# Performance work log

Hardware: AMD Instinct MI355X
Metric: run time of the kernel (lower is better)

## Reference

```python
import jax, jax.numpy as jnp
import numpy as np

NUM_HEADS = 4
EPS = 1e-12  # torch F.normalize eps


def _l2norm(t):
    # normalize along last axis, matching torch.nn.functional.normalize
    n = jnp.sqrt(jnp.sum(t * t, axis=-1, keepdims=True))
    return t / jnp.maximum(n, EPS)


def setup_inputs() -> dict:
    key = jax.random.key(0)
    k1, k2 = jax.random.split(key)
    B, N, C = 4, 8192, 768
    x = jax.random.normal(k1, (B, N, C), dtype=jnp.float32)
    W_qkvv = jax.random.normal(k2, (3 * C, C), dtype=jnp.float32) * (C ** -0.5)
    temperature = jnp.ones((NUM_HEADS, 1, 1), dtype=jnp.float32)
    return {"x": x, "W_qkvv": W_qkvv, "temperature": temperature}


def reference(x, W_qkvv, temperature):
    B, N, C = x.shape
    H = NUM_HEADS
    D = C // H
    # qkvv projection: [B,N,3C] -> [3,B,H,N,D]
    qkvv = (x @ W_qkvv.T).reshape(B, N, 3, H, D).transpose(2, 0, 3, 1, 4)
    q, k, v = qkvv[0], qkvv[1], qkvv[2]        # each [B,H,N,D]
    q = jnp.swapaxes(q, -2, -1)                # [B,H,D,N]
    k = jnp.swapaxes(k, -2, -1)                # [B,H,D,N]
    v = jnp.swapaxes(v, -2, -1)                # [B,H,D,N]
    q = _l2norm(q)
    k = _l2norm(k)
    # channel attention scores: [B,H,D,D], temperature broadcast per head
    attn = jnp.einsum('bhdn,bhen->bhde', q, k) * temperature[None]
    attn = jax.nn.softmax(attn, axis=-1)
    # dropout is identity in eval mode
    x_CA = jnp.einsum('bhde,bhen->bhdn', attn, v)   # [B,H,D,N]
    out = x_CA.transpose(0, 3, 1, 2).reshape(B, N, C)
    return out
```

## Files before the change

### kernel.cpp

```cpp
#include <hip/hip_runtime.h>
#include <hip/hip_bf16.h>
#include <cstddef>
#include <cstdint>

#define B_   4
#define N_   8192
#define C_   768
#define H_   4
#define D_   192
#define CQ_  2304
#define M_   32768

typedef __attribute__((ext_vector_type(8))) short short8_t;
typedef __attribute__((ext_vector_type(4))) float f32x4;

typedef const __attribute__((address_space(1))) uint gq_uint;
typedef __attribute__((address_space(3))) uint lds_uint;

__device__ inline ushort f2bf(float f){
  uint u = __float_as_uint(f);
  u += 0x7FFFu + ((u >> 16) & 1u);
  return (ushort)(u >> 16);
}
__device__ inline float bf2f(ushort u){ return __uint_as_float(((uint)u) << 16); }

__global__ __launch_bounds__(256) void cvt_all(const float* __restrict__ x,
                                               ushort* __restrict__ xb,
                                               const float* __restrict__ Wq,
                                               ushort* __restrict__ Wb,
                                               float* __restrict__ norm2){
  int i = blockIdx.x * 256 + threadIdx.x;
  if (i < 6144) norm2[i] = 0.f;
  if (i < 6291456){
    float4 v = ((const float4*)x)[i];
    ushort4 o;
    o.x = f2bf(v.x); o.y = f2bf(v.y); o.z = f2bf(v.z); o.w = f2bf(v.w);
    ((ushort4*)xb)[i] = o;
  } else if (i < 6291456 + 442368){
    int j = i - 6291456;
    float4 v = ((const float4*)Wq)[j];
    ushort4 o;
    o.x = f2bf(v.x); o.y = f2bf(v.y); o.z = f2bf(v.z); o.w = f2bf(v.w);
    ((ushort4*)Wb)[j] = o;
  }
}

__global__ __launch_bounds__(512, 4) void gemm_qkvv(const ushort* __restrict__ A,
                                                    const ushort* __restrict__ W,
                                                    ushort* __restrict__ Cq,
                                                    float* __restrict__ norm2){
  extern __shared__ ushort lds[];
  const int t = threadIdx.x;
  const int bid = blockIdx.x;
  const int wg  = (bid & 7) * 288 + (bid >> 3);
  const int by = wg / 9, bx = wg % 9;
  const int m0 = by * 128, n0 = bx * 256;
  const int wid = t >> 6, lane = t & 63;
  const int wr = wid >> 2, wc = wid & 3;
  const int lr = lane & 15, lg = lane >> 4;
  const int srow4  = lane >> 2;
  const int sslot4 = (lane & 3) ^ ((lane >> 4) & 3);
  const int slx = (lg ^ ((lr >> 2) & 3)) * 8;

  f32x4 acc[4][4];
  #pragma unroll
  for (int i = 0; i < 4; ++i)
    #pragma unroll
    for (int j = 0; j < 4; ++j)
      acc[i][j] = (f32x4){0.f, 0.f, 0.f, 0.f};

  #define STAGE_A(KT, LBASE)                                                    \
    __builtin_amdgcn_global_load_lds(                                           \
        (gq_uint*)(const void*)(A + (size_t)(m0 + wid*16 + srow4) * 768         \
                                + (KT) * 32 + sslot4 * 8),                      \
        (lds_uint*)(void*)((LBASE) + wid * 512), 16, 0, 0);

  #define STAGE_W(KT, LBASE)                                                    \
    _Pragma("unroll")                                                           \
    for (int r_ = 0; r_ < 2; ++r_){                                             \
      __builtin_amdgcn_global_load_lds(                                         \
          (gq_uint*)(const void*)(W + (size_t)(n0 + r_*128 + wid*16 + srow4) * 768 \
                                  + (KT) * 32 + sslot4 * 8),                    \
          (lds_uint*)(void*)((LBASE) + r_*4096 + wid * 512), 16, 0, 0);         \
    }

  #define RD_A(DST)                                                             \
    _Pragma("unroll") for (int fm = 0; fm < 4; ++fm)                            \
      DST[fm] = *(const short8_t*)(bA + (wr*64 + fm*16 + lr) * 32 + slx);

  #define RD_B(DST)                                                             \
    _Pragma("unroll") for (int fn = 0; fn < 4; ++fn)                            \
      DST[fn] = *(const short8_t*)(bB + (wc*64 + fn*16 + lr) * 32 + slx);

  #define MM(AR, BR)                                                            \
    __builtin_amdgcn_s_setprio(1);                                              \
    _Pragma("unroll") for (int fm = 0; fm < 4; ++fm)                            \
    _Pragma("unroll") for (int fn = 0; fn < 4; ++fn)                            \
      acc[fm][fn] = __builtin_amdgcn_mfma_f32_16x16x32_bf16(                    \
          AR[fm], BR[fn], acc[fm][fn], 0, 0, 0);                                \
    __builtin_amdgcn_s_setprio(0);

  STAGE_A(0, lds);          STAGE_W(0, lds + 4096);
  STAGE_A(1, lds + 12288);  STAGE_W(1, lds + 12288 + 4096);
  asm volatile("s_waitcnt vmcnt(3)" ::: "memory");
  __builtin_amdgcn_s_barrier();
  __builtin_amdgcn_sched_barrier(0);

  short8_t af[4], bf[4];

  #pragma unroll 2
  for (int kt = 0; kt < 22; ++kt){
    const ushort* bA = lds + (kt & 1) * 12288;
    const ushort* bB = bA + 4096;
    ushort* nA = lds + (kt & 1) * 12288;
    RD_A(af); RD_B(bf);
    asm volatile("s_waitcnt lgkmcnt(0)" ::: "memory");
    __builtin_amdgcn_sched_barrier(0);
    __builtin_amdgcn_s_barrier();
    __builtin_amdgcn_sched_barrier(0);
    STAGE_A(kt + 2, nA);
    STAGE_W(kt + 2, nA + 4096);
    MM(af, bf);
    asm volatile("s_waitcnt vmcnt(3)" ::: "memory");
    __builtin_amdgcn_s_barrier();
    __builtin_amdgcn_sched_barrier(0);
  }
  {
    const ushort* bA = lds;
    const ushort* bB = bA + 4096;
    RD_A(af); RD_B(bf);
    asm volatile("s_waitcnt lgkmcnt(0)" ::: "memory");
    __builtin_amdgcn_sched_barrier(0);
    MM(af, bf);
    asm volatile("s_waitcnt vmcnt(0)" ::: "memory");
    __builtin_amdgcn_s_barrier();
    __builtin_amdgcn_sched_barrier(0);
  }
  {
    const ushort* bA = lds + 12288;
    const ushort* bB = bA + 4096;
    RD_A(af); RD_B(bf);
    asm volatile("s_waitcnt lgkmcnt(0)" ::: "memory");
    __builtin_amdgcn_sched_barrier(0);
    MM(af, bf);
  }
  #undef STAGE_A
  #undef STAGE_W
  #undef RD_A
  #undef RD_B
  #undef MM

  #pragma unroll
  for (int fm = 0; fm < 4; ++fm)
    #pragma unroll
    for (int fn = 0; fn < 4; ++fn)
      #pragma unroll
      for (int r = 0; r < 4; ++r){
        int m = m0 + wr*64 + fm*16 + lg*4 + r;
        int c = n0 + wc*64 + fn*16 + lr;
        Cq[(size_t)m * CQ_ + c] = f2bf(acc[fm][fn][r]);
      }

  if (bx < 6){
    const int b = m0 >> 13;
    #pragma unroll
    for (int fn = 0; fn < 4; ++fn){
      float s = 0.f;
      #pragma unroll
      for (int fm = 0; fm < 4; ++fm)
        #pragma unroll
        for (int r = 0; r < 4; ++r)
          s = fmaf(acc[fm][fn][r], acc[fm][fn][r], s);
      s += __shfl_xor(s, 16);
      s += __shfl_xor(s, 32);
      if (lg == 0)
        atomicAdd(&norm2[b * 1536 + n0 + wc*64 + fn*16 + lr], s);
    }
  }
}

__global__ __launch_bounds__(512) void gram_mfma(const ushort* __restrict__ Qk,
                                                 float* __restrict__ Sp){
  const int kc = blockIdx.x;
  const int bh = blockIdx.y;
  const int b = bh >> 2, h = bh & 3;
  __shared__ __align__(16) uint pk[2][2][3232];
  const int t = threadIdx.x;
  const int wid = t >> 6, lane = t & 63;
  const int wd = wid >> 2, we = wid & 3;
  const int lr = lane & 15, lg = lane >> 4;

  f32x4 acc[6][3];
  #pragma unroll
  for (int i = 0; i < 6; ++i)
    #pragma unroll
    for (int j = 0; j < 3; ++j)
      acc[i][j] = (f32x4){0.f, 0.f, 0.f, 0.f};

  const uint* gq = (const uint*)Qk + (size_t)b * N_ * 1152;

  uint r0[6], r1[6];
  #define GLOAD(IT)                                                             \
    _Pragma("unroll") for (int u = 0; u < 6; ++u){                              \
      int id = u*512 + t, mat = id/1536, rem = id - mat*1536;                   \
      int np = rem/96, c = rem - np*96;                                         \
      const uint* p = gq + (size_t)(kc*512 + (IT)*32 + 2*np)*1152               \
                         + (mat ? 384 + h*96 : h*96) + c;                       \
      r0[u] = p[0]; r1[u] = p[1152];                                            \
    }
  #define LWRITE(BUF)                                                           \
    _Pragma("unroll") for (int u = 0; u < 6; ++u){                              \
      int id = u*512 + t, mat = id/1536, rem = id - mat*1536;                   \
      int np = rem/96, c = rem - np*96;                                         \
      uint o0 = (r0[u] & 0xFFFFu) | (r1[u] << 16);                              \
      uint o1 = (r0[u] >> 16) | (r1[u] & 0xFFFF0000u);                          \
      *(uint2*)&pk[BUF][mat][np*202 + 2*c] = (uint2){o0, o1};                   \
    }

  GLOAD(0);
  LWRITE(0);
  __syncthreads();

  for (int it = 0; it < 16; ++it){
    const int cur = it & 1;
    if (it < 15) GLOAD(it + 1);
    union { uint u[4]; short8_t v; } af[6], bf[3];
    #pragma unroll
    for (int i = 0; i < 6; ++i){
      int d = wd * 96 + i * 16 + lr;
      #pragma unroll
      for (int p = 0; p < 4; ++p)
        af[i].u[p] = pk[cur][0][(lg*4 + p)*202 + d];
    }
    #pragma unroll
    for (int j = 0; j < 3; ++j){
      int e = we * 48 + j * 16 + lr;
      #pragma unroll
      for (int p = 0; p < 4; ++p)
        bf[j].u[p] = pk[cur][1][(lg*4 + p)*202 + e];
    }
    #pragma unroll
    for (int i = 0; i < 6; ++i)
      #pragma unroll
      for (int j = 0; j < 3; ++j)
        acc[i][j] = __builtin_amdgcn_mfma_f32_16x16x32_bf16(af[i].v, bf[j].v, acc[i][j], 0, 0, 0);
    if (it < 15) LWRITE(cur ^ 1);
    __syncthreads();
  }
  #undef GLOAD
  #undef LWRITE

  float* base = Sp + (size_t)(kc * 16 + bh) * 192 * 192;
  #pragma unroll
  for (int i = 0; i < 6; ++i)
    #pragma unroll
    for (int j = 0; j < 3; ++j)
      #pragma unroll
      for (int r = 0; r < 4; ++r){
        int d = wd * 96 + i * 16 + lg * 4 + r;
        int e = we * 48 + j * 16 + lr;
        base[(size_t)d * 192 + e] = acc[i][j][r];
      }
}

__global__ __launch_bounds__(256) void softmax_k(const float* __restrict__ Sp,
                                                 const float* __restrict__ norm2,
                                                 const float* __restrict__ temp,
                                                 ushort* __restrict__ attn){
  const int wid  = blockIdx.x * 4 + (threadIdx.x >> 6);
  const int lane = threadIdx.x & 63;
  const int bh = wid / 192, d = wid % 192;
  const int b = bh >> 2, h = bh & 3;
  const float nq = sqrtf(norm2[b*1536 + h*192 + d]);
  const float sc = temp[h] / fmaxf(nq, 1e-12f);
  const float* Sr = Sp + ((size_t)bh * 192 + d) * 192;
  float l[3];
  #pragma unroll
  for (int u = 0; u < 3; ++u){
    int e = lane + u * 64;
    float s = 0.f;
    #pragma unroll
    for (int kc = 0; kc < 16; ++kc)
      s += Sr[(size_t)kc * (16*192*192) + e];
    float nk = sqrtf(norm2[b*1536 + 768 + h*192 + e]);
    l[u] = s * sc / fmaxf(nk, 1e-12f);
  }
  float m = fmaxf(l[0], fmaxf(l[1], l[2]));
  #pragma unroll
  for (int off = 32; off; off >>= 1) m = fmaxf(m, __shfl_xor(m, off));
  float p[3], s = 0.f;
  #pragma unroll
  for (int u = 0; u < 3; ++u){ p[u] = expf(l[u] - m); s += p[u]; }
  #pragma unroll
  for (int off = 32; off; off >>= 1) s += __shfl_xor(s, off);
  float inv = 1.f / s;
  ushort* ar = attn + ((size_t)bh * 192 + d) * 192;
  #pragma unroll
  for (int u = 0; u < 3; ++u) ar[lane + u*64] = f2bf(p[u] * inv);
}

__global__ __launch_bounds__(256) void out_gemm(const ushort* __restrict__ Q,
                                                const ushort* __restrict__ attn,
                                                float* __restrict__ out){
  const int bh = blockIdx.y;
  const int b = bh >> 2, h = bh & 3;
  const int n0 = blockIdx.x * 128;
  const int t = threadIdx.x, w = t >> 6, lane = t & 63;
  const int wn = w & 1, wd = w >> 1;
  const int lr = lane & 15, lg = lane >> 4;
  f32x4 acc[4][6];
  #pragma unroll
  for (int i = 0; i < 4; ++i)
    #pragma unroll
    for (int j = 0; j < 6; ++j)
      acc[i][j] = (f32x4){0.f, 0.f, 0.f, 0.f};

  const ushort* Vbase = Q + 1536 + h * 192;
  const ushort* Abase = attn + (size_t)bh * 192 * 192;

  #pragma unroll
  for (int kk = 0; kk < 6; ++kk){
    const int e = kk * 32 + lg * 8;
    short8_t av[4], bv[6];
    #pragma unroll
    for (int f = 0; f < 4; ++f){
      int n = n0 + wn*64 + f*16 + lr;
      av[f] = *(const short8_t*)(Vbase + (size_t)(b*N_ + n) * CQ_ + e);
    }
    #pragma unroll
    for (int f = 0; f < 6; ++f){
      int d = wd*96 + f*16 + lr;
      bv[f] = *(const short8_t*)(Abase + d * 192 + e);
    }
    #pragma unroll
    for (int i = 0; i < 4; ++i)
      #pragma unroll
      for (int j = 0; j < 6; ++j)
        acc[i][j] = __builtin_amdgcn_mfma_f32_16x16x32_bf16(av[i], bv[j], acc[i][j], 0, 0, 0);
  }
  #pragma unroll
  for (int i = 0; i < 4; ++i)
    #pragma unroll
    for (int j = 0; j < 6; ++j)
      #pragma unroll
      for (int r = 0; r < 4; ++r){
        int n = n0 + wn*64 + i*16 + lg*4 + r;
        int c = h*192 + wd*96 + j*16 + lr;
        out[(size_t)(b*N_ + n) * 768 + c] = acc[i][j][r];
      }
}

extern "C" void kernel_launch(void* const* d_in, const int* in_sizes, int n_in,
                              void* d_out, int out_size, void* d_ws, size_t ws_size,
                              hipStream_t stream){
  const float* x    = (const float*)d_in[0];
  const float* Wq   = (const float*)d_in[1];
  const float* temp = (const float*)d_in[2];
  float* out = (float*)d_out;
  char* ws = (char*)d_ws;

  ushort* xb    = (ushort*)(ws + 0);
  float*  S_part= (float*)(ws + 0);
  ushort* attn  = (ushort*)(ws + 37748736);
  ushort* Wb    = (ushort*)(ws + 50331648);
  ushort* qkvv  = (ushort*)(ws + 53870592);
  float*  norm2 = (float*)(ws + 204865536);

  static_assert(sizeof(ushort) == 2, "");
  hipFuncSetAttribute((const void*)gemm_qkvv,
                      hipFuncAttributeMaxDynamicSharedMemorySize, 49152);

  cvt_all<<<26304, 256, 0, stream>>>(x, xb, Wq, Wb, norm2);

  gemm_qkvv<<<2304, 512, 49152, stream>>>(xb, Wb, qkvv, norm2);

  gram_mfma<<<dim3(16, 16), 512, 0, stream>>>(qkvv, S_part);
  softmax_k<<<768, 256, 0, stream>>>(S_part, norm2, temp, attn);
  out_gemm<<<dim3(64, 16), 256, 0, stream>>>(qkvv, attn, out);
}
```

Measured before the change: 238.5 us.

## Retile QKV GEMM to 128x128 tiles with 4 waves and K=64 steps

Reshapes the QKV projection GEMM from 128x256 output tiles with 8 waves and K-step 32 to 128x128 tiles with 4 waves, each computing 64x64, and K-step 64. The LDS layout moves to 64-element rows with an XOR swizzle, double-buffered in 64 KB. Each barrier now covers twice as many MFMAs, and the grid doubles to 4608 blocks. In exchange, arithmetic intensity per tile drops, and the larger LDS footprint may limit how many blocks fit on a CU.

```diff
diff --git a/kernel.cpp b/kernel.cpp
--- a/kernel.cpp
+++ b/kernel.cpp
@@ -45,22 +45,21 @@
   }
 }
 
-__global__ __launch_bounds__(512, 4) void gemm_qkvv(const ushort* __restrict__ A,
+__global__ __launch_bounds__(256, 2) void gemm_qkvv(const ushort* __restrict__ A,
                                                     const ushort* __restrict__ W,
                                                     ushort* __restrict__ Cq,
                                                     float* __restrict__ norm2){
   extern __shared__ ushort lds[];
   const int t = threadIdx.x;
   const int bid = blockIdx.x;
-  const int wg  = (bid & 7) * 288 + (bid >> 3);
-  const int by = wg / 9, bx = wg % 9;
-  const int m0 = by * 128, n0 = bx * 256;
+  const int wg  = (bid & 7) * 576 + (bid >> 3);
+  const int by = wg / 18, bx = wg % 18;
+  const int m0 = by * 128, n0 = bx * 128;
   const int wid = t >> 6, lane = t & 63;
-  const int wr = wid >> 2, wc = wid & 3;
+  const int wm = wid >> 1, wn = wid & 1;
   const int lr = lane & 15, lg = lane >> 4;
-  const int srow4  = lane >> 2;
-  const int sslot4 = (lane & 3) ^ ((lane >> 4) & 3);
-  const int slx = (lg ^ ((lr >> 2) & 3)) * 8;
+  const int srow  = lane >> 3;
+  const int sslot = (lane & 7) ^ srow;
 
   f32x4 acc[4][4];
   #pragma unroll
@@ -69,65 +68,67 @@
     for (int j = 0; j < 4; ++j)
       acc[i][j] = (f32x4){0.f, 0.f, 0.f, 0.f};
 
-  #define STAGE_A(KT, LBASE)                                                    \
-    __builtin_amdgcn_global_load_lds(                                           \
-        (gq_uint*)(const void*)(A + (size_t)(m0 + wid*16 + srow4) * 768         \
-                                + (KT) * 32 + sslot4 * 8),                      \
-        (lds_uint*)(void*)((LBASE) + wid * 512), 16, 0, 0);
-
-  #define STAGE_W(KT, LBASE)                                                    \
+  #define STAGE_M(GPTR, G0, KT, LBASE)                                          \
     _Pragma("unroll")                                                           \
-    for (int r_ = 0; r_ < 2; ++r_){                                             \
+    for (int rnd_ = 0; rnd_ < 4; ++rnd_){                                       \
+      const int row_ = wid * 32 + rnd_ * 8;                                     \
       __builtin_amdgcn_global_load_lds(                                         \
-          (gq_uint*)(const void*)(W + (size_t)(n0 + r_*128 + wid*16 + srow4) * 768 \
-                                  + (KT) * 32 + sslot4 * 8),                    \
-          (lds_uint*)(void*)((LBASE) + r_*4096 + wid * 512), 16, 0, 0);         \
+          (gq_uint*)(const void*)((GPTR) + (size_t)((G0) + row_ + srow) * 768   \
+                                  + (KT) * 64 + sslot * 8),                     \
+          (lds_uint*)(void*)((LBASE) + row_ * 64), 16, 0, 0);                   \
     }
 
   #define RD_A(DST)                                                             \
-    _Pragma("unroll") for (int fm = 0; fm < 4; ++fm)                            \
-      DST[fm] = *(const short8_t*)(bA + (wr*64 + fm*16 + lr) * 32 + slx);
+    _Pragma("unroll") for (int kk = 0; kk < 2; ++kk){                           \
+      const int sl = ((kk * 4 + lg) ^ (lr & 7)) * 8;                            \
+      _Pragma("unroll") for (int fm = 0; fm < 4; ++fm)                          \
+        DST[kk][fm] = *(const short8_t*)(bA + (wm*64 + fm*16 + lr)*64 + sl); }
 
   #define RD_B(DST)                                                             \
-    _Pragma("unroll") for (int fn = 0; fn < 4; ++fn)                            \
-      DST[fn] = *(const short8_t*)(bB + (wc*64 + fn*16 + lr) * 32 + slx);
+    _Pragma("unroll") for (int kk = 0; kk < 2; ++kk){                           \
+      const int sl = ((kk * 4 + lg) ^ (lr & 7)) * 8;                            \
+      _Pragma("unroll") for (int fn = 0; fn < 4; ++fn)                          \
+        DST[kk][fn] = *(const short8_t*)(bB + (wn*64 + fn*16 + lr)*64 + sl); }
 
   #define MM(AR, BR)                                                            \
     __builtin_amdgcn_s_setprio(1);                                              \
+    _Pragma("unroll") for (int kk = 0; kk < 2; ++kk)                            \
     _Pragma("unroll") for (int fm = 0; fm < 4; ++fm)                            \
     _Pragma("unroll") for (int fn = 0; fn < 4; ++fn)                            \
       acc[fm][fn] = __builtin_amdgcn_mfma_f32_16x16x32_bf16(                    \
-          AR[fm], BR[fn], acc[fm][fn], 0, 0, 0);                                \
+          AR[kk][fm], BR[kk][fn], acc[fm][fn], 0, 0, 0);                        \
     __builtin_amdgcn_s_setprio(0);
 
-  STAGE_A(0, lds);          STAGE_W(0, lds + 4096);
-  STAGE_A(1, lds + 12288);  STAGE_W(1, lds + 12288 + 4096);
-  asm volatile("s_waitcnt vmcnt(3)" ::: "memory");
+  STAGE_M(A, m0, 0, lds);
+  STAGE_M(W, n0, 0, lds + 8192);
+  STAGE_M(A, m0, 1, lds + 16384);
+  STAGE_M(W, n0, 1, lds + 16384 + 8192);
+  asm volatile("s_waitcnt vmcnt(8)" ::: "memory");
   __builtin_amdgcn_s_barrier();
   __builtin_amdgcn_sched_barrier(0);
 
-  short8_t af[4], bf[4];
+  short8_t af[2][4], bf[2][4];
 
   #pragma unroll 2
-  for (int kt = 0; kt < 22; ++kt){
-    const ushort* bA = lds + (kt & 1) * 12288;
-    const ushort* bB = bA + 4096;
-    ushort* nA = lds + (kt & 1) * 12288;
+  for (int kt = 0; kt < 10; ++kt){
+    const ushort* bA = lds + (kt & 1) * 16384;
+    const ushort* bB = bA + 8192;
+    ushort* nb = lds + (kt & 1) * 16384;
     RD_A(af); RD_B(bf);
     asm volatile("s_waitcnt lgkmcnt(0)" ::: "memory");
     __builtin_amdgcn_sched_barrier(0);
     __builtin_amdgcn_s_barrier();
     __builtin_amdgcn_sched_barrier(0);
-    STAGE_A(kt + 2, nA);
-    STAGE_W(kt + 2, nA + 4096);
+    STAGE_M(A, m0, kt + 2, nb);
+    STAGE_M(W, n0, kt + 2, nb + 8192);
     MM(af, bf);
-    asm volatile("s_waitcnt vmcnt(3)" ::: "memory");
+    asm volatile("s_waitcnt vmcnt(8)" ::: "memory");
     __builtin_amdgcn_s_barrier();
     __builtin_amdgcn_sched_barrier(0);
   }
   {
     const ushort* bA = lds;
-    const ushort* bB = bA + 4096;
+    const ushort* bB = bA + 8192;
     RD_A(af); RD_B(bf);
     asm volatile("s_waitcnt lgkmcnt(0)" ::: "memory");
     __builtin_amdgcn_sched_barrier(0);
@@ -137,15 +138,14 @@
     __builtin_amdgcn_sched_barrier(0);
   }
   {
-    const ushort* bA = lds + 12288;
-    const ushort* bB = bA + 4096;
+    const ushort* bA = lds + 16384;
+    const ushort* bB = bA + 8192;
     RD_A(af); RD_B(bf);
     asm volatile("s_waitcnt lgkmcnt(0)" ::: "memory");
     __builtin_amdgcn_sched_barrier(0);
     MM(af, bf);
   }
-  #undef STAGE_A
-  #undef STAGE_W
+  #undef STAGE_M
   #undef RD_A
   #undef RD_B
   #undef MM
@@ -156,12 +156,12 @@
     for (int fn = 0; fn < 4; ++fn)
       #pragma unroll
       for (int r = 0; r < 4; ++r){
-        int m = m0 + wr*64 + fm*16 + lg*4 + r;
-        int c = n0 + wc*64 + fn*16 + lr;
+        int m = m0 + wm*64 + fm*16 + lg*4 + r;
+        int c = n0 + wn*64 + fn*16 + lr;
         Cq[(size_t)m * CQ_ + c] = f2bf(acc[fm][fn][r]);
       }
 
-  if (bx < 6){
+  if (bx < 12){
     const int b = m0 >> 13;
     #pragma unroll
     for (int fn = 0; fn < 4; ++fn){
@@ -174,7 +174,7 @@
       s += __shfl_xor(s, 16);
       s += __shfl_xor(s, 32);
       if (lg == 0)
-        atomicAdd(&norm2[b * 1536 + n0 + wc*64 + fn*16 + lr], s);
+        atomicAdd(&norm2[b * 1536 + n0 + wn*64 + fn*16 + lr], s);
     }
   }
 }
@@ -368,11 +368,11 @@
 
   static_assert(sizeof(ushort) == 2, "");
   hipFuncSetAttribute((const void*)gemm_qkvv,
-                      hipFuncAttributeMaxDynamicSharedMemorySize, 49152);
+                      hipFuncAttributeMaxDynamicSharedMemorySize, 65536);
 
   cvt_all<<<26304, 256, 0, stream>>>(x, xb, Wq, Wb, norm2);
 
-  gemm_qkvv<<<2304, 512, 49152, stream>>>(xb, Wb, qkvv, norm2);
+  gemm_qkvv<<<4608, 256, 65536, stream>>>(xb, Wb, qkvv, norm2);
 
   gram_mfma<<<dim3(16, 16), 512, 0, stream>>>(qkvv, S_part);
   softmax_k<<<768, 256, 0, stream>>>(S_part, norm2, temp, attn);
```

After: 232.6 us. 1.03x faster.
